# Kernel optimization log

Hardware: AMD Instinct MI355X
Metric: run time of the kernel (lower is better)

The kernel has to match this reference:

```python
import jax, jax.numpy as jnp
import numpy as np


def setup_inputs() -> dict:
    key = jax.random.key(0)
    k1, k2, k3 = jax.random.split(key, 3)
    B, C, W, H, K = 8, 3, 512, 512, 13
    Wo, Ho = W - K + 1, H - K + 1
    return {
        "img": jax.random.normal(k1, (B, C, W, H), dtype=jnp.float32),
        "hori": jax.random.normal(k2, (B, K, Wo, Ho), dtype=jnp.float32),
        "vert": jax.random.normal(k3, (B, K, Wo, Ho), dtype=jnp.float32),
        "kernel_size": K,
    }


def reference(img, hori, vert, kernel_size):
    # out[b,c,i,j] = sum_{u,v} img[b,c,i+u,j+v] * vert[b,u,i,j] * hori[b,v,i,j]
    K = kernel_size
    B, C, W, H = img.shape
    Wo, Ho = W - K + 1, H - K + 1
    out = jnp.zeros((B, C, Wo, Ho), img.dtype)
    # Fixed small K x K loop over kernel taps; all pixel/batch dims vectorized.
    for v in range(K):
        h_v = hori[:, v][:, None]  # [B,1,Wo,Ho]
        acc = jnp.zeros((B, C, Wo, Ho), img.dtype)
        for u in range(K):
            acc = acc + img[:, :, u:u + Wo, v:v + Ho] * vert[:, u][:, None]
        out = out + acc * h_v
    return out
```

## Files before the change

kernel.cpp:

```cpp
#include <hip/hip_runtime.h>


#define KK 13
#define NB 8
#define NC 3
#define IW 512
#define IH 512
#define WO 500
#define HO 500
#define QROW 125
#define NT 384
#define NQ (KK * QROW)

typedef __attribute__((address_space(1))) const void g_void;
typedef __attribute__((address_space(3))) void l_void;

__global__ __launch_bounds__(NT) void sepconv_kernel(
    const float* __restrict__ img,
    const float* __restrict__ hori,
    const float* __restrict__ vert,
    float* __restrict__ out)
{
    __shared__ float4 s_vert[NQ];
    __shared__ float4 s_hori[NQ];

    const int tid = threadIdx.y * 128 + threadIdx.x;
    const int i = blockIdx.x;
    const int b = blockIdx.y;

    const size_t khw = (size_t)WO * HO;
    const size_t rs4 = khw / 4;
    const float4* vsrc = (const float4*)(vert + (size_t)b * KK * khw + (size_t)i * HO);
    const float4* hsrc = (const float4*)(hori + (size_t)b * KK * khw + (size_t)i * HO);

    #pragma unroll
    for (int f0 = 0; f0 < NQ; f0 += NT) {
        const int f = f0 + tid;
        if (f < NQ) {
            const unsigned u = (unsigned)f / QROW;
            const unsigned q = (unsigned)f - u * QROW;
            __builtin_amdgcn_global_load_lds(
                (g_void*)(vsrc + (size_t)u * rs4 + q),
                (l_void*)&s_vert[f], 16, 0, 0);
            __builtin_amdgcn_global_load_lds(
                (g_void*)(hsrc + (size_t)u * rs4 + q),
                (l_void*)&s_hori[f], 16, 0, 0);
        }
    }
    __syncthreads();

    const int tj = threadIdx.x;
    const int c  = threadIdx.y;
    if (tj >= QROW) return;
    const int j0 = tj * 4;

    const float* ibase = img + (((size_t)(b * NC + c) * IW) + i) * IH + j0;

    float tmp[4][KK];
    #pragma unroll
    for (int jq = 0; jq < 4; ++jq)
        #pragma unroll
        for (int v = 0; v < KK; ++v)
            tmp[jq][v] = 0.0f;

    float4 c0 = *(const float4*)(ibase + 0);
    float4 c1 = *(const float4*)(ibase + 4);
    float4 c2 = *(const float4*)(ibase + 8);
    float4 c3 = *(const float4*)(ibase + 12);

    #pragma unroll
    for (int u = 0; u < KK; ++u) {
        float4 n0, n1, n2, n3;
        if (u < KK - 1) {
            const float* rp = ibase + (size_t)(u + 1) * IH;
            n0 = *(const float4*)(rp + 0);
            n1 = *(const float4*)(rp + 4);
            n2 = *(const float4*)(rp + 8);
            n3 = *(const float4*)(rp + 12);
        }

        const float4 vt = s_vert[u * QROW + tj];

        float row[16];
        row[0]  = c0.x; row[1]  = c0.y; row[2]  = c0.z; row[3]  = c0.w;
        row[4]  = c1.x; row[5]  = c1.y; row[6]  = c1.z; row[7]  = c1.w;
        row[8]  = c2.x; row[9]  = c2.y; row[10] = c2.z; row[11] = c2.w;
        row[12] = c3.x; row[13] = c3.y; row[14] = c3.z; row[15] = c3.w;

        #pragma unroll
        for (int v = 0; v < KK; ++v) {
            tmp[0][v] += row[0 + v] * vt.x;
            tmp[1][v] += row[1 + v] * vt.y;
            tmp[2][v] += row[2 + v] * vt.z;
            tmp[3][v] += row[3 + v] * vt.w;
        }

        if (u < KK - 1) {
            c0 = n0; c1 = n1; c2 = n2; c3 = n3;
        }
    }

    float4 o = make_float4(0.f, 0.f, 0.f, 0.f);
    #pragma unroll
    for (int v = 0; v < KK; ++v) {
        const float4 hv = s_hori[v * QROW + tj];
        o.x += tmp[0][v] * hv.x;
        o.y += tmp[1][v] * hv.y;
        o.z += tmp[2][v] * hv.z;
        o.w += tmp[3][v] * hv.w;
    }

    float* op = out + (((size_t)(b * NC + c) * WO) + i) * HO + j0;
    *(float4*)op = o;
}

extern "C" void kernel_launch(void* const* d_in, const int* in_sizes, int n_in,
                              void* d_out, int out_size, void* d_ws, size_t ws_size,
                              hipStream_t stream) {
    const float* img  = (const float*)d_in[0];
    const float* hori = (const float*)d_in[1];
    const float* vert = (const float*)d_in[2];
    float* out = (float*)d_out;

    dim3 block(128, 3, 1);
    dim3 grid(WO, NB, 1);
    hipLaunchKernelGGL(sepconv_kernel, grid, block, 0, stream, img, hori, vert, out);
}
```

Measured before the change: 267.8 us.

## Make sepconv persistent with double-buffered LDS staging of filter rows

Replaces the one-block-per-output-row grid with a persistent grid of 768 blocks that loop over half-row tasks. Each block prefetches the next task's vert/hori rows into a second LDS buffer with async global-to-LDS loads while it computes the current task. The goal is to hide the filter-staging latency and cut block launch overhead. In exchange the block shrinks to 64x3 threads, fewer waves are resident, and the waits emitted at the barrier may serialize the prefetch with the image loads.

Result: slower. 307.9 us (+15.0%).

```diff
diff --git a/kernel.cpp b/kernel.cpp
--- a/kernel.cpp
+++ b/kernel.cpp
@@ -8,9 +8,15 @@
 #define IH 512
 #define WO 500
 #define HO 500
+#define KHW 250000
+#define RS4 62500
 #define QROW 125
-#define NT 384
-#define NQ (KK * QROW)
+#define NTX 64
+#define NTY 3
+#define NT 192
+#define SLOT (KK * 64)
+#define NTASK (NB * 2 * WO)
+#define NBLK 768
 
 typedef __attribute__((address_space(1))) const void g_void;
 typedef __attribute__((address_space(3))) void l_void;
@@ -21,97 +27,118 @@
     const float* __restrict__ vert,
     float* __restrict__ out)
 {
-    __shared__ float4 s_vert[NQ];
-    __shared__ float4 s_hori[NQ];
+    __shared__ float4 smem[2][2][SLOT];
 
-    const int tid = threadIdx.y * 128 + threadIdx.x;
-    const int i = blockIdx.x;
-    const int b = blockIdx.y;
+    const int tx = threadIdx.x;
+    const int ty = threadIdx.y;
+    const int tid = ty * NTX + tx;
 
-    const size_t khw = (size_t)WO * HO;
-    const size_t rs4 = khw / 4;
-    const float4* vsrc = (const float4*)(vert + (size_t)b * KK * khw + (size_t)i * HO);
-    const float4* hsrc = (const float4*)(hori + (size_t)b * KK * khw + (size_t)i * HO);
+    auto stage = [&](int t, int sb) {
+        const unsigned bb   = (unsigned)t / 1000u;
+        const unsigned rem  = (unsigned)t - bb * 1000u;
+        const unsigned half = rem / 500u;
+        const unsigned ii   = rem - half * 500u;
+        const size_t base = (size_t)bb * KK * KHW + (size_t)ii * HO + half * 256;
+        const float4* v4 = (const float4*)(vert + base);
+        const float4* h4 = (const float4*)(hori + base);
+        const int qlim = half ? 61 : 64;
+        #pragma unroll
+        for (int f0 = 0; f0 < SLOT; f0 += NT) {
+            const int f = f0 + tid;
+            if (f < SLOT) {
+                const int u = f >> 6;
+                const int q = f & 63;
+                if (q < qlim) {
+                    __builtin_amdgcn_global_load_lds(
+                        (g_void*)(v4 + (size_t)u * RS4 + q),
+                        (l_void*)&smem[sb][0][f], 16, 0, 0);
+                    __builtin_amdgcn_global_load_lds(
+                        (g_void*)(h4 + (size_t)u * RS4 + q),
+                        (l_void*)&smem[sb][1][f], 16, 0, 0);
+                }
+            }
+        }
+    };
 
-    #pragma unroll
-    for (int f0 = 0; f0 < NQ; f0 += NT) {
-        const int f = f0 + tid;
-        if (f < NQ) {
-            const unsigned u = (unsigned)f / QROW;
-            const unsigned q = (unsigned)f - u * QROW;
-            __builtin_amdgcn_global_load_lds(
-                (g_void*)(vsrc + (size_t)u * rs4 + q),
-                (l_void*)&s_vert[f], 16, 0, 0);
-            __builtin_amdgcn_global_load_lds(
-                (g_void*)(hsrc + (size_t)u * rs4 + q),
-                (l_void*)&s_hori[f], 16, 0, 0);
-        }
-    }
-    __syncthreads();
+    int t = blockIdx.x;
+    int s = 0;
+    stage(t, 0);
 
-    const int tj = threadIdx.x;
-    const int c  = threadIdx.y;
-    if (tj >= QROW) return;
-    const int j0 = tj * 4;
+    while (t < NTASK) {
+        const int nt = t + NBLK;
+        __syncthreads();
+        if (nt < NTASK) stage(nt, s ^ 1);
 
-    const float* ibase = img + (((size_t)(b * NC + c) * IW) + i) * IH + j0;
+        const unsigned bb   = (unsigned)t / 1000u;
+        const unsigned rem  = (unsigned)t - bb * 1000u;
+        const unsigned half = rem / 500u;
+        const unsigned ii   = rem - half * 500u;
+        const int tj = (int)half * 64 + tx;
+        if (tj < QROW) {
+            const int j0 = tj * 4;
+            const float* ibase = img + (((size_t)(bb * NC + ty) * IW) + ii) * IH + j0;
 
-    float tmp[4][KK];
-    #pragma unroll
-    for (int jq = 0; jq < 4; ++jq)
-        #pragma unroll
-        for (int v = 0; v < KK; ++v)
-            tmp[jq][v] = 0.0f;
+            float tmp[4][KK];
+            #pragma unroll
+            for (int jq = 0; jq < 4; ++jq)
+                #pragma unroll
+                for (int v = 0; v < KK; ++v)
+                    tmp[jq][v] = 0.0f;
 
-    float4 c0 = *(const float4*)(ibase + 0);
-    float4 c1 = *(const float4*)(ibase + 4);
-    float4 c2 = *(const float4*)(ibase + 8);
-    float4 c3 = *(const float4*)(ibase + 12);
+            float4 c0 = *(const float4*)(ibase + 0);
+            float4 c1 = *(const float4*)(ibase + 4);
+            float4 c2 = *(const float4*)(ibase + 8);
+            float4 c3 = *(const float4*)(ibase + 12);
 
-    #pragma unroll
-    for (int u = 0; u < KK; ++u) {
-        float4 n0, n1, n2, n3;
-        if (u < KK - 1) {
-            const float* rp = ibase + (size_t)(u + 1) * IH;
-            n0 = *(const float4*)(rp + 0);
-            n1 = *(const float4*)(rp + 4);
-            n2 = *(const float4*)(rp + 8);
-            n3 = *(const float4*)(rp + 12);
+            #pragma unroll
+            for (int u = 0; u < KK; ++u) {
+                float4 n0, n1, n2, n3;
+                if (u < KK - 1) {
+                    const float* rp = ibase + (size_t)(u + 1) * IH;
+                    n0 = *(const float4*)(rp + 0);
+                    n1 = *(const float4*)(rp + 4);
+                    n2 = *(const float4*)(rp + 8);
+                    n3 = *(const float4*)(rp + 12);
+                }
+
+                const float4 vt = smem[s][0][u * 64 + tx];
+
+                float row[16];
+                row[0]  = c0.x; row[1]  = c0.y; row[2]  = c0.z; row[3]  = c0.w;
+                row[4]  = c1.x; row[5]  = c1.y; row[6]  = c1.z; row[7]  = c1.w;
+                row[8]  = c2.x; row[9]  = c2.y; row[10] = c2.z; row[11] = c2.w;
+                row[12] = c3.x; row[13] = c3.y; row[14] = c3.z; row[15] = c3.w;
+
+                #pragma unroll
+                for (int v = 0; v < KK; ++v) {
+                    tmp[0][v] += row[0 + v] * vt.x;
+                    tmp[1][v] += row[1 + v] * vt.y;
+                    tmp[2][v] += row[2 + v] * vt.z;
+                    tmp[3][v] += row[3 + v] * vt.w;
+                }
+
+                if (u < KK - 1) {
+                    c0 = n0; c1 = n1; c2 = n2; c3 = n3;
+                }
+            }
+
+            float4 o = make_float4(0.f, 0.f, 0.f, 0.f);
+            #pragma unroll
+            for (int v = 0; v < KK; ++v) {
+                const float4 hv = smem[s][1][v * 64 + tx];
+                o.x += tmp[0][v] * hv.x;
+                o.y += tmp[1][v] * hv.y;
+                o.z += tmp[2][v] * hv.z;
+                o.w += tmp[3][v] * hv.w;
+            }
+
+            float* op = out + (((size_t)(bb * NC + ty) * WO) + ii) * HO + j0;
+            *(float4*)op = o;
         }
 
-        const float4 vt = s_vert[u * QROW + tj];
-
-        float row[16];
-        row[0]  = c0.x; row[1]  = c0.y; row[2]  = c0.z; row[3]  = c0.w;
-        row[4]  = c1.x; row[5]  = c1.y; row[6]  = c1.z; row[7]  = c1.w;
-        row[8]  = c2.x; row[9]  = c2.y; row[10] = c2.z; row[11] = c2.w;
-        row[12] = c3.x; row[13] = c3.y; row[14] = c3.z; row[15] = c3.w;
-
-        #pragma unroll
-        for (int v = 0; v < KK; ++v) {
-            tmp[0][v] += row[0 + v] * vt.x;
-            tmp[1][v] += row[1 + v] * vt.y;
-            tmp[2][v] += row[2 + v] * vt.z;
-            tmp[3][v] += row[3 + v] * vt.w;
-        }
-
-        if (u < KK - 1) {
-            c0 = n0; c1 = n1; c2 = n2; c3 = n3;
-        }
+        t = nt;
+        s ^= 1;
     }
-
-    float4 o = make_float4(0.f, 0.f, 0.f, 0.f);
-    #pragma unroll
-    for (int v = 0; v < KK; ++v) {
-        const float4 hv = s_hori[v * QROW + tj];
-        o.x += tmp[0][v] * hv.x;
-        o.y += tmp[1][v] * hv.y;
-        o.z += tmp[2][v] * hv.z;
-        o.w += tmp[3][v] * hv.w;
-    }
-
-    float* op = out + (((size_t)(b * NC + c) * WO) + i) * HO + j0;
-    *(float4*)op = o;
 }
 
 extern "C" void kernel_launch(void* const* d_in, const int* in_sizes, int n_in,
@@ -122,7 +149,7 @@
     const float* vert = (const float*)d_in[2];
     float* out = (float*)d_out;
 
-    dim3 block(128, 3, 1);
-    dim3 grid(WO, NB, 1);
+    dim3 block(NTX, NTY, 1);
+    dim3 grid(NBLK, 1, 1);
     hipLaunchKernelGGL(sepconv_kernel, grid, block, 0, stream, img, hori, vert, out);
 }
```

## Remap work to per-wave tasks with channel loop and no block barrier

Applied to the files above, without the earlier changes.

Each wave now owns one (batch, row, half-row) task and loops over the three channels, instead of one thread per channel within a block sharing a row. vert is staged into a per-wave LDS slot and synchronised with a waitcnt rather than a block barrier, and hori is read directly from global memory in the epilogue. This removes the 128-wide blocks with 3 idle lanes per wave and the __syncthreads. In exchange, work that was spread over three channel threads is now serial within one thread, and the second half-row wave has many inactive lanes (only 61 of 64 are valid).

After: 336.0 us. 1.25x slower.

```diff
diff --git a/kernel.cpp b/kernel.cpp
--- a/kernel.cpp
+++ b/kernel.cpp
@@ -8,9 +8,14 @@
 #define IH 512
 #define WO 500
 #define HO 500
+#define KHW 250000
+#define RS4 62500
 #define QROW 125
 #define NT 384
-#define NQ (KK * QROW)
+#define WPB 6
+#define SLOT (KK * 64)
+#define NTASK (NB * 2 * WO)
+#define NBLK ((NTASK + WPB - 1) / WPB)
 
 typedef __attribute__((address_space(1))) const void g_void;
 typedef __attribute__((address_space(3))) void l_void;
@@ -21,97 +26,99 @@
     const float* __restrict__ vert,
     float* __restrict__ out)
 {
-    __shared__ float4 s_vert[NQ];
-    __shared__ float4 s_hori[NQ];
+    __shared__ float4 smem[WPB * SLOT];
 
-    const int tid = threadIdx.y * 128 + threadIdx.x;
-    const int i = blockIdx.x;
-    const int b = blockIdx.y;
+    const int wave = threadIdx.x >> 6;
+    const int lane = threadIdx.x & 63;
+    const int W = blockIdx.x * WPB + wave;
+    if (W >= NTASK) return;
 
-    const size_t khw = (size_t)WO * HO;
-    const size_t rs4 = khw / 4;
-    const float4* vsrc = (const float4*)(vert + (size_t)b * KK * khw + (size_t)i * HO);
-    const float4* hsrc = (const float4*)(hori + (size_t)b * KK * khw + (size_t)i * HO);
+    const unsigned bb   = (unsigned)W / 1000u;
+    const unsigned rem  = (unsigned)W - bb * 1000u;
+    const unsigned half = rem / 500u;
+    const unsigned ii   = rem - half * 500u;
+    const int q = (int)half * 64 + lane;
+    const bool valid = q < QROW;
 
-    #pragma unroll
-    for (int f0 = 0; f0 < NQ; f0 += NT) {
-        const int f = f0 + tid;
-        if (f < NQ) {
-            const unsigned u = (unsigned)f / QROW;
-            const unsigned q = (unsigned)f - u * QROW;
+    float4* slot = &smem[wave * SLOT];
+
+    const float4* vsrc = (const float4*)(vert + (size_t)bb * KK * KHW + (size_t)ii * HO);
+    const float4* hsrc = (const float4*)(hori + (size_t)bb * KK * KHW + (size_t)ii * HO);
+
+    if (valid) {
+        #pragma unroll
+        for (int u = 0; u < KK; ++u)
             __builtin_amdgcn_global_load_lds(
-                (g_void*)(vsrc + (size_t)u * rs4 + q),
-                (l_void*)&s_vert[f], 16, 0, 0);
-            __builtin_amdgcn_global_load_lds(
-                (g_void*)(hsrc + (size_t)u * rs4 + q),
-                (l_void*)&s_hori[f], 16, 0, 0);
+                (g_void*)(vsrc + (size_t)u * RS4 + q),
+                (l_void*)&slot[u * 64 + lane], 16, 0, 0);
+    }
+    __builtin_amdgcn_s_waitcnt(0x0f70);
+
+    if (valid) {
+        const int j0 = q * 4;
+
+        #pragma unroll 1
+        for (int c = 0; c < NC; ++c) {
+            const float* ibase = img + (((size_t)(bb * NC + c) * IW) + ii) * IH + j0;
+
+            float tmp[4][KK];
+            #pragma unroll
+            for (int jq = 0; jq < 4; ++jq)
+                #pragma unroll
+                for (int v = 0; v < KK; ++v)
+                    tmp[jq][v] = 0.0f;
+
+            float4 c0 = *(const float4*)(ibase + 0);
+            float4 c1 = *(const float4*)(ibase + 4);
+            float4 c2 = *(const float4*)(ibase + 8);
+            float4 c3 = *(const float4*)(ibase + 12);
+
+            #pragma unroll
+            for (int u = 0; u < KK; ++u) {
+                float4 n0, n1, n2, n3;
+                if (u < KK - 1) {
+                    const float* rp = ibase + (size_t)(u + 1) * IH;
+                    n0 = *(const float4*)(rp + 0);
+                    n1 = *(const float4*)(rp + 4);
+                    n2 = *(const float4*)(rp + 8);
+                    n3 = *(const float4*)(rp + 12);
+                }
+
+                const float4 vt = slot[u * 64 + lane];
+
+                float row[16];
+                row[0]  = c0.x; row[1]  = c0.y; row[2]  = c0.z; row[3]  = c0.w;
+                row[4]  = c1.x; row[5]  = c1.y; row[6]  = c1.z; row[7]  = c1.w;
+                row[8]  = c2.x; row[9]  = c2.y; row[10] = c2.z; row[11] = c2.w;
+                row[12] = c3.x; row[13] = c3.y; row[14] = c3.z; row[15] = c3.w;
+
+                #pragma unroll
+                for (int v = 0; v < KK; ++v) {
+                    tmp[0][v] += row[0 + v] * vt.x;
+                    tmp[1][v] += row[1 + v] * vt.y;
+                    tmp[2][v] += row[2 + v] * vt.z;
+                    tmp[3][v] += row[3 + v] * vt.w;
+                }
+
+                if (u < KK - 1) {
+                    c0 = n0; c1 = n1; c2 = n2; c3 = n3;
+                }
+            }
+
+            float4 o = make_float4(0.f, 0.f, 0.f, 0.f);
+            #pragma unroll
+            for (int v = 0; v < KK; ++v) {
+                const float4 hv = hsrc[(size_t)v * RS4 + q];
+                o.x += tmp[0][v] * hv.x;
+                o.y += tmp[1][v] * hv.y;
+                o.z += tmp[2][v] * hv.z;
+                o.w += tmp[3][v] * hv.w;
+            }
+
+            float* op = out + (((size_t)(bb * NC + c) * WO) + ii) * HO + j0;
+            *(float4*)op = o;
         }
     }
-    __syncthreads();
-
-    const int tj = threadIdx.x;
-    const int c  = threadIdx.y;
-    if (tj >= QROW) return;
-    const int j0 = tj * 4;
-
-    const float* ibase = img + (((size_t)(b * NC + c) * IW) + i) * IH + j0;
-
-    float tmp[4][KK];
-    #pragma unroll
-    for (int jq = 0; jq < 4; ++jq)
-        #pragma unroll
-        for (int v = 0; v < KK; ++v)
-            tmp[jq][v] = 0.0f;
-
-    float4 c0 = *(const float4*)(ibase + 0);
-    float4 c1 = *(const float4*)(ibase + 4);
-    float4 c2 = *(const float4*)(ibase + 8);
-    float4 c3 = *(const float4*)(ibase + 12);
-
-    #pragma unroll
-    for (int u = 0; u < KK; ++u) {
-        float4 n0, n1, n2, n3;
-        if (u < KK - 1) {
-            const float* rp = ibase + (size_t)(u + 1) * IH;
-            n0 = *(const float4*)(rp + 0);
-            n1 = *(const float4*)(rp + 4);
-            n2 = *(const float4*)(rp + 8);
-            n3 = *(const float4*)(rp + 12);
-        }
-
-        const float4 vt = s_vert[u * QROW + tj];
-
-        float row[16];
-        row[0]  = c0.x; row[1]  = c0.y; row[2]  = c0.z; row[3]  = c0.w;
-        row[4]  = c1.x; row[5]  = c1.y; row[6]  = c1.z; row[7]  = c1.w;
-        row[8]  = c2.x; row[9]  = c2.y; row[10] = c2.z; row[11] = c2.w;
-        row[12] = c3.x; row[13] = c3.y; row[14] = c3.z; row[15] = c3.w;
-
-        #pragma unroll
-        for (int v = 0; v < KK; ++v) {
-            tmp[0][v] += row[0 + v] * vt.x;
-            tmp[1][v] += row[1 + v] * vt.y;
-            tmp[2][v] += row[2 + v] * vt.z;
-            tmp[3][v] += row[3 + v] * vt.w;
-        }
-
-        if (u < KK - 1) {
-            c0 = n0; c1 = n1; c2 = n2; c3 = n3;
-        }
-    }
-
-    float4 o = make_float4(0.f, 0.f, 0.f, 0.f);
-    #pragma unroll
-    for (int v = 0; v < KK; ++v) {
-        const float4 hv = s_hori[v * QROW + tj];
-        o.x += tmp[0][v] * hv.x;
-        o.y += tmp[1][v] * hv.y;
-        o.z += tmp[2][v] * hv.z;
-        o.w += tmp[3][v] * hv.w;
-    }
-
-    float* op = out + (((size_t)(b * NC + c) * WO) + i) * HO + j0;
-    *(float4*)op = o;
 }
 
 extern "C" void kernel_launch(void* const* d_in, const int* in_sizes, int n_in,
@@ -122,7 +129,7 @@
     const float* vert = (const float*)d_in[2];
     float* out = (float*)d_out;
 
-    dim3 block(128, 3, 1);
-    dim3 grid(WO, NB, 1);
+    dim3 block(NT, 1, 1);
+    dim3 grid(NBLK, 1, 1);
     hipLaunchKernelGGL(sepconv_kernel, grid, block, 0, stream, img, hori, vert, out);
 }
```
